# Kernel optimization log

Measured on AMD Instinct MI355X. Metric: run time of the kernel, lower is better.

The kernel has to match this reference:

```python
import jax, jax.numpy as jnp
import numpy as np

B, D_IMG, D_TXT, E = 4096, 768, 768, 512
LAMBDA_CMP = 1.0
EPS = 1e-10


def setup_inputs() -> dict:
    key = jax.random.key(0)
    k1, k2, k3, k4, k5 = jax.random.split(key, 5)
    return {
        "images": jax.random.normal(k1, (B, D_IMG), dtype=jnp.float32),
        "texts": jax.random.normal(k2, (B, D_TXT), dtype=jnp.float32),
        "labels": jax.random.randint(k3, (B,), 0, 1000, dtype=jnp.int32),
        "W_img": jax.random.normal(k4, (D_IMG, E), dtype=jnp.float32) / np.sqrt(D_IMG),
        "W_txt": jax.random.normal(k5, (D_TXT, E), dtype=jnp.float32) / np.sqrt(D_TXT),
        "logit_scale": jnp.asarray(np.log(1.0 / 0.07), dtype=jnp.float32),
    }


def reference(images, texts, labels, W_img, W_txt, logit_scale):
    # CLIP-style encoders: linear project + L2 normalize
    img = images @ W_img
    txt = texts @ W_txt
    img = img / jnp.linalg.norm(img, axis=-1, keepdims=True)
    txt = txt / jnp.linalg.norm(txt, axis=-1, keepdims=True)
    logits = jnp.exp(logit_scale) * (img @ txt.T)  # [B, B]

    b = logits.shape[0]
    rows = jnp.arange(b)
    logp = jax.nn.log_softmax(logits, axis=-1)
    clip_loss = -jnp.mean(logp[rows, labels])

    probs = jnp.exp(logp)                # softmax probs [B, B]
    p_yi = probs[rows, labels]           # [B]
    # columns j whose label differs from sample i's label AND prob exceeds p_yi
    diff_label = labels[None, :] != labels[:, None]           # [B, B]
    mask = diff_label & (probs > p_yi[:, None])               # [B, B]
    denom = jnp.sum(jnp.where(mask, probs, 0.0), axis=1)      # [B]
    has_any = jnp.any(mask, axis=1)
    cmp_loss = jnp.sum(jnp.where(has_any, p_yi / (denom + EPS), 0.0)) / b

    return clip_loss + LAMBDA_CMP * cmp_loss
```

## Files before the change

kernel.cpp:

```cpp
#include <hip/hip_runtime.h>
#include <stdint.h>

#define BATCH 4096
#define DDIM  768
#define EDIM  512
#define NS    64
#define LOG2E 1.44269504088896340736f

using short8  = __attribute__((ext_vector_type(8))) short;
using float4v = __attribute__((ext_vector_type(4))) float;

__device__ __forceinline__ unsigned short f2bf(float x) {
    union { float f; uint32_t u; } v; v.f = x;
    uint32_t u = v.u;
    u += 0x7FFFu + ((u >> 16) & 1u);
    return (unsigned short)(u >> 16);
}
__device__ __forceinline__ float bf2f(unsigned short h) {
    union { uint32_t u; float f; } v; v.u = ((uint32_t)h) << 16;
    return v.f;
}

__device__ __forceinline__ void gl2lds16(const void* g, void* l) {
    __builtin_amdgcn_global_load_lds(
        (const __attribute__((address_space(1))) void*)g,
        (__attribute__((address_space(3))) void*)l, 16, 0, 0);
}

__global__ void prep(const float* __restrict__ images, const float* __restrict__ texts,
                     const float* __restrict__ W_img, const float* __restrict__ W_txt,
                     unsigned short* __restrict__ img_bf, unsigned short* __restrict__ txt_bf,
                     unsigned short* __restrict__ wt_img, unsigned short* __restrict__ wt_txt) {
    __shared__ float tile[32][33];
    int bid = blockIdx.x;
    if (bid < 6144) {
        int which = bid >= 3072;
        int i = (bid - (which ? 3072 : 0)) * 256 + threadIdx.x;
        const float* in = which ? texts : images;
        unsigned short* out = which ? txt_bf : img_bf;
        float4 v = ((const float4*)in)[i];
        ushort4 o;
        o.x = f2bf(v.x); o.y = f2bf(v.y); o.z = f2bf(v.z); o.w = f2bf(v.w);
        ((ushort4*)out)[i] = o;
        return;
    }
    int tb = bid - 6144;
    int which = tb >= 384;
    if (which) tb -= 384;
    const float* W = which ? W_txt : W_img;
    unsigned short* Wt = which ? wt_txt : wt_img;
    int n0 = (tb & 15) * 32, k0 = (tb >> 4) * 32;
    int tid = threadIdx.x;
    for (int p = 0; p < 4; ++p) {
        int e = tid + p * 256; int lr = e >> 5, lc = e & 31;
        tile[lc][lr] = W[(size_t)(k0 + lr) * EDIM + n0 + lc];
    }
    __syncthreads();
    for (int p = 0; p < 4; ++p) {
        int e = tid + p * 256; int lr = e >> 5, lc = e & 31;
        Wt[(size_t)(n0 + lr) * DDIM + k0 + lc] = f2bf(tile[lr][lc]);
    }
}

__global__ __launch_bounds__(256) void gemm_nt(const unsigned short* __restrict__ Aimg,
                                               const unsigned short* __restrict__ Atxt,
                                               const unsigned short* __restrict__ Bimg,
                                               const unsigned short* __restrict__ Btxt,
                                               unsigned short* __restrict__ Cimg,
                                               unsigned short* __restrict__ Ctxt) {
    const unsigned short* A  = blockIdx.z ? Atxt : Aimg;
    const unsigned short* Bm = blockIdx.z ? Btxt : Bimg;
    unsigned short* C        = blockIdx.z ? Ctxt : Cimg;
    __shared__ __align__(16) unsigned short As[2][128 * 64];
    __shared__ __align__(16) unsigned short Bs[2][64 * 64];
    int tid = threadIdx.x;
    int wave = tid >> 6, lane = tid & 63;
    int q = lane >> 4, r = lane & 15;
    int m0 = blockIdx.x * 128, n0 = blockIdx.y * 64;
    int sw = (r >> 1) & 3;

    const unsigned short* gsA[4];
    unsigned short* lsA[4];
    for (int i = 0; i < 4; ++i) {
        int u = i * 256 + tid;
        int kc2 = u >> 9, row = (u >> 2) & 127, kq = u & 3;
        int kq2 = kq ^ ((row >> 1) & 3);
        gsA[i] = &A[(size_t)(m0 + row) * DDIM + kc2 * 32 + kq2 * 8];
        lsA[i] = &As[0][u * 8];
    }
    const unsigned short* gsB[2];
    unsigned short* lsB[2];
    for (int i = 0; i < 2; ++i) {
        int u = i * 256 + tid;
        int kc2 = u >> 8, row = (u >> 2) & 63, kq = u & 3;
        int kq2 = kq ^ ((row >> 1) & 3);
        gsB[i] = &Bm[(size_t)(n0 + row) * DDIM + kc2 * 32 + kq2 * 8];
        lsB[i] = &Bs[0][u * 8];
    }

    float4v acc[2][4];
    for (int a = 0; a < 2; ++a)
        for (int t = 0; t < 4; ++t) acc[a][t] = (float4v){0.f, 0.f, 0.f, 0.f};

    for (int i = 0; i < 4; ++i) gl2lds16(gsA[i], lsA[i]);
    for (int i = 0; i < 2; ++i) gl2lds16(gsB[i], lsB[i]);
    __syncthreads();

    for (int it = 0; it < DDIM / 64; ++it) {
        int b = it & 1;
        if (it < DDIM / 64 - 1) {
            int k0 = (it + 1) * 64;
            for (int i = 0; i < 4; ++i) gl2lds16(gsA[i] + k0, lsA[i] + (b ^ 1) * (128 * 64));
            for (int i = 0; i < 2; ++i) gl2lds16(gsB[i] + k0, lsB[i] + (b ^ 1) * (64 * 64));
        }
        for (int kc2 = 0; kc2 < 2; ++kc2) {
            short8 a0 = *(const short8*)&As[b][kc2 * 4096 + (wave * 32 + r) * 32 + (q ^ sw) * 8];
            short8 a1 = *(const short8*)&As[b][kc2 * 4096 + (wave * 32 + 16 + r) * 32 + (q ^ sw) * 8];
            for (int t = 0; t < 4; ++t) {
                short8 bfr = *(const short8*)&Bs[b][kc2 * 2048 + (t * 16 + r) * 32 + (q ^ sw) * 8];
                acc[0][t] = __builtin_amdgcn_mfma_f32_16x16x32_bf16(a0, bfr, acc[0][t], 0, 0, 0);
                acc[1][t] = __builtin_amdgcn_mfma_f32_16x16x32_bf16(a1, bfr, acc[1][t], 0, 0, 0);
            }
        }
        __syncthreads();
    }
    for (int rg = 0; rg < 2; ++rg)
        for (int t = 0; t < 4; ++t)
            for (int g = 0; g < 4; ++g)
                C[(size_t)(m0 + wave * 32 + rg * 16 + q * 4 + g) * EDIM + n0 + t * 16 + r] =
                    f2bf(acc[rg][t][g]);
}

__global__ void norm_rows(unsigned short* __restrict__ Pa, unsigned short* __restrict__ Pb) {
    unsigned short* P = blockIdx.y ? Pb : Pa;
    int wave = threadIdx.x >> 6, lane = threadIdx.x & 63;
    int row = blockIdx.x * 4 + wave;
    unsigned short* p = &P[(size_t)row * 512 + lane * 8];
    union { unsigned short us[8]; uint4 u4; } v;
    v.u4 = *(const uint4*)p;
    float f[8], s = 0.f;
    for (int j = 0; j < 8; ++j) { f[j] = bf2f(v.us[j]); s += f[j] * f[j]; }
    for (int off = 1; off < 64; off <<= 1) s += __shfl_xor(s, off);
    float rn = rsqrtf(s);
    for (int j = 0; j < 8; ++j) v.us[j] = f2bf(f[j] * rn);
    *(uint4*)p = v.u4;
}

__global__ void tdot(const unsigned short* __restrict__ img, const unsigned short* __restrict__ txt,
                     const int* __restrict__ labels, float* __restrict__ tout) {
    int wave = threadIdx.x >> 6, lane = threadIdx.x & 63;
    int row = blockIdx.x * 4 + wave;
    int lab = labels[row];
    union { unsigned short us[8]; uint4 u4; } a, b;
    a.u4 = *(const uint4*)&img[(size_t)row * 512 + lane * 8];
    b.u4 = *(const uint4*)&txt[(size_t)lab * 512 + lane * 8];
    float s = 0.f;
    for (int j = 0; j < 8; ++j) s += bf2f(a.us[j]) * bf2f(b.us[j]);
    for (int off = 1; off < 64; off <<= 1) s += __shfl_xor(s, off);
    if (lane == 0) tout[row] = s;
}

__global__ __launch_bounds__(256) void flash_pass(
    const unsigned short* __restrict__ img, const unsigned short* __restrict__ txt,
    const int* __restrict__ labels, const float* __restrict__ tvals,
    const float* __restrict__ ls,
    float* __restrict__ lP, float* __restrict__ dP) {
    __shared__ __align__(16) unsigned short As[2][128 * 64];
    __shared__ __align__(16) unsigned short Bs[2][128 * 64];
    int tid = threadIdx.x;
    int wave = tid >> 6, lane = tid & 63;
    int wr = wave >> 1, wc = wave & 1;
    int q = lane >> 4, r = lane & 15;
    int n0 = blockIdx.x * 128;
    int m0 = blockIdx.y * 128;
    float alpha = expf(ls[0]);
    float c1 = alpha * LOG2E;
    int sw = (r >> 1) & 3;

    const unsigned short* gsA[4]; const unsigned short* gsB[4];
    unsigned short *lsA[4], *lsB[4];
    for (int i = 0; i < 4; ++i) {
        int u = i * 256 + tid;
        int kc2 = u >> 9, row = (u >> 2) & 127, kq = u & 3;
        int kq2 = kq ^ ((row >> 1) & 3);
        gsA[i] = &img[(size_t)(m0 + row) * 512 + kc2 * 32 + kq2 * 8];
        gsB[i] = &txt[(size_t)(n0 + row) * 512 + kc2 * 32 + kq2 * 8];
        lsA[i] = &As[0][u * 8];
        lsB[i] = &Bs[0][u * 8];
    }

    float4v acc[4][4];
    #pragma unroll
    for (int st = 0; st < 4; ++st)
        #pragma unroll
        for (int cf = 0; cf < 4; ++cf) acc[st][cf] = (float4v){0.f, 0.f, 0.f, 0.f};

    for (int i = 0; i < 4; ++i) gl2lds16(gsA[i], lsA[i]);
    for (int i = 0; i < 4; ++i) gl2lds16(gsB[i], lsB[i]);
    __syncthreads();

    for (int it = 0; it < 8; ++it) {
        int b = it & 1;
        if (it < 7) {
            int k0 = (it + 1) * 64;
            for (int i = 0; i < 4; ++i) gl2lds16(gsA[i] + k0, lsA[i] + (b ^ 1) * (128 * 64));
            for (int i = 0; i < 4; ++i) gl2lds16(gsB[i] + k0, lsB[i] + (b ^ 1) * (128 * 64));
        }
        #pragma unroll
        for (int kc2 = 0; kc2 < 2; ++kc2) {
            short8 av[4], bv[4];
            #pragma unroll
            for (int st = 0; st < 4; ++st)
                av[st] = *(const short8*)&As[b][kc2 * 4096 + (wr * 64 + st * 16 + r) * 32 + (q ^ sw) * 8];
            #pragma unroll
            for (int cf = 0; cf < 4; ++cf)
                bv[cf] = *(const short8*)&Bs[b][kc2 * 4096 + (wc * 64 + cf * 16 + r) * 32 + (q ^ sw) * 8];
            #pragma unroll
            for (int st = 0; st < 4; ++st)
                #pragma unroll
                for (int cf = 0; cf < 4; ++cf)
                    acc[st][cf] = __builtin_amdgcn_mfma_f32_16x16x32_bf16(av[st], bv[cf],
                                                                          acc[st][cf], 0, 0, 0);
        }
        __syncthreads();
    }

    int lc[4];
    #pragma unroll
    for (int cf = 0; cf < 4; ++cf) lc[cf] = labels[n0 + wc * 64 + cf * 16 + r];
    int cb = blockIdx.x * 2 + wc;
    #pragma unroll
    for (int st = 0; st < 4; ++st) {
        int labr[4]; float tr[4];
        #pragma unroll
        for (int g = 0; g < 4; ++g) {
            int rw = m0 + wr * 64 + st * 16 + q * 4 + g;
            labr[g] = labels[rw];
            tr[g] = tvals[rw];
        }
        float l4[4] = {0.f, 0.f, 0.f, 0.f}, d4[4] = {0.f, 0.f, 0.f, 0.f};
        #pragma unroll
        for (int cf = 0; cf < 4; ++cf)
            #pragma unroll
            for (int g = 0; g < 4; ++g) {
                float a = acc[st][cf][g];
                float p = exp2f(fmaf(a, c1, -c1));
                l4[g] += p;
                d4[g] += ((a > tr[g]) && (lc[cf] != labr[g])) ? p : 0.f;
            }
        #pragma unroll
        for (int g = 0; g < 4; ++g) {
            float lv = l4[g], dv = d4[g];
            for (int off = 1; off < 16; off <<= 1) {
                lv += __shfl_xor(lv, off);
                dv += __shfl_xor(dv, off);
            }
            if (r == 0) {
                int rw = m0 + wr * 64 + st * 16 + q * 4 + g;
                lP[(size_t)rw * NS + cb] = lv;
                dP[(size_t)rw * NS + cb] = dv;
            }
        }
    }
}

__global__ void combine(const float* __restrict__ lP, const float* __restrict__ dP,
                        const float* __restrict__ tvals, const float* __restrict__ ls,
                        float* __restrict__ out) {
    int row = blockIdx.x * 256 + threadIdx.x;
    float alpha = expf(ls[0]);
    float L = 0.f, D = 0.f;
    for (int s = 0; s < NS; ++s) {
        L += lP[(size_t)row * NS + s];
        D += dP[(size_t)row * NS + s];
    }
    float tm = alpha * (tvals[row] - 1.0f);
    float clip = logf(L) - tm;
    float py = expf(tm) / L;
    float cmp = (D > 0.f) ? py / (D / L + 1e-10f) : 0.f;
    float v = clip + cmp;
    for (int off = 1; off < 64; off <<= 1) v += __shfl_xor(v, off);
    __shared__ float w4[4];
    int wave = threadIdx.x >> 6, lane = threadIdx.x & 63;
    if (lane == 0) w4[wave] = v;
    __syncthreads();
    if (threadIdx.x == 0)
        atomicAdd(out, (w4[0] + w4[1] + w4[2] + w4[3]) * (1.0f / BATCH));
}

extern "C" void kernel_launch(void* const* d_in, const int* in_sizes, int n_in,
                              void* d_out, int out_size, void* d_ws, size_t ws_size,
                              hipStream_t stream) {
    const float* images = (const float*)d_in[0];
    const float* texts  = (const float*)d_in[1];
    const int*   labels = (const int*)d_in[2];
    const float* W_img  = (const float*)d_in[3];
    const float* W_txt  = (const float*)d_in[4];
    const float* lscale = (const float*)d_in[5];
    float* out = (float*)d_out;

    char* ws = (char*)d_ws;
    unsigned short* img_bf = (unsigned short*)(ws + 0);
    unsigned short* txt_bf = (unsigned short*)(ws + 6291456);
    unsigned short* wt_img = (unsigned short*)(ws + 12582912);
    unsigned short* wt_txt = (unsigned short*)(ws + 13369344);
    unsigned short* proj_i = (unsigned short*)(ws + 14155776);
    unsigned short* proj_t = (unsigned short*)(ws + 18350080);
    float*          lP     = (float*)(ws + 0);
    float*          dP     = (float*)(ws + 1048576);
    float*          tvals  = (float*)(ws + 2097152);

    hipMemsetAsync(out, 0, sizeof(float), stream);
    prep<<<6912, 256, 0, stream>>>(images, texts, W_img, W_txt, img_bf, txt_bf, wt_img, wt_txt);
    gemm_nt<<<dim3(BATCH / 128, EDIM / 64, 2), 256, 0, stream>>>(img_bf, txt_bf, wt_img, wt_txt,
                                                                 proj_i, proj_t);
    norm_rows<<<dim3(BATCH / 4, 2), 256, 0, stream>>>(proj_i, proj_t);
    tdot<<<BATCH / 4, 256, 0, stream>>>(proj_i, proj_t, labels, tvals);
    flash_pass<<<dim3(BATCH / 128, BATCH / 128), 256, 0, stream>>>(proj_i, proj_t, labels, tvals,
                                                                   lscale, lP, dP);
    combine<<<16, 256, 0, stream>>>(lP, dP, tvals, lscale, out);
}
```

Before: 141.0 us.

## Enlarge flash_pass tile to 256x256 with 8 waves and interleaved prefetch schedule

Grows the logits tile per block from 128x128 to 256x256 and the block from 4 to 8 waves, so each wave now accumulates a 128x64 output slice. The K loop is split into four MFMA phases, each with its own LDS fragment loads, part of the next-tile global-to-LDS prefetch, explicit barriers and raised wave priority. The aim is more reuse per LDS byte and better overlap of memory traffic with MFMA work. The cost is 128KB of LDS per block and a grid of only 256 blocks, which allows one block per CU and gives no tail slack.

```diff
diff --git a/kernel.cpp b/kernel.cpp
--- a/kernel.cpp
+++ b/kernel.cpp
@@ -160,81 +160,154 @@
     if (lane == 0) tout[row] = s;
 }
 
-__global__ __launch_bounds__(256) void flash_pass(
+__global__ __launch_bounds__(512) void flash_pass(
     const unsigned short* __restrict__ img, const unsigned short* __restrict__ txt,
     const int* __restrict__ labels, const float* __restrict__ tvals,
     const float* __restrict__ ls,
     float* __restrict__ lP, float* __restrict__ dP) {
-    __shared__ __align__(16) unsigned short As[2][128 * 64];
-    __shared__ __align__(16) unsigned short Bs[2][128 * 64];
+    __shared__ __align__(16) unsigned short As[2][16384];
+    __shared__ __align__(16) unsigned short Bs[2][16384];
     int tid = threadIdx.x;
     int wave = tid >> 6, lane = tid & 63;
-    int wr = wave >> 1, wc = wave & 1;
+    int wr = wave >> 2, wc = wave & 3;
     int q = lane >> 4, r = lane & 15;
-    int n0 = blockIdx.x * 128;
-    int m0 = blockIdx.y * 128;
+    int n0 = blockIdx.x * 256;
+    int m0 = blockIdx.y * 256;
     float alpha = expf(ls[0]);
     float c1 = alpha * LOG2E;
     int sw = (r >> 1) & 3;
 
-    const unsigned short* gsA[4]; const unsigned short* gsB[4];
-    unsigned short *lsA[4], *lsB[4];
+    int soff[4], slds[4];
     for (int i = 0; i < 4; ++i) {
-        int u = i * 256 + tid;
-        int kc2 = u >> 9, row = (u >> 2) & 127, kq = u & 3;
+        int u = i * 512 + tid;
+        int kc2 = u >> 10, row = (u >> 2) & 255, kq = u & 3;
         int kq2 = kq ^ ((row >> 1) & 3);
-        gsA[i] = &img[(size_t)(m0 + row) * 512 + kc2 * 32 + kq2 * 8];
-        gsB[i] = &txt[(size_t)(n0 + row) * 512 + kc2 * 32 + kq2 * 8];
-        lsA[i] = &As[0][u * 8];
-        lsB[i] = &Bs[0][u * 8];
-    }
-
-    float4v acc[4][4];
-    #pragma unroll
-    for (int st = 0; st < 4; ++st)
-        #pragma unroll
-        for (int cf = 0; cf < 4; ++cf) acc[st][cf] = (float4v){0.f, 0.f, 0.f, 0.f};
-
-    for (int i = 0; i < 4; ++i) gl2lds16(gsA[i], lsA[i]);
-    for (int i = 0; i < 4; ++i) gl2lds16(gsB[i], lsB[i]);
-    __syncthreads();
-
-    for (int it = 0; it < 8; ++it) {
-        int b = it & 1;
-        if (it < 7) {
-            int k0 = (it + 1) * 64;
-            for (int i = 0; i < 4; ++i) gl2lds16(gsA[i] + k0, lsA[i] + (b ^ 1) * (128 * 64));
-            for (int i = 0; i < 4; ++i) gl2lds16(gsB[i] + k0, lsB[i] + (b ^ 1) * (128 * 64));
-        }
-        #pragma unroll
-        for (int kc2 = 0; kc2 < 2; ++kc2) {
-            short8 av[4], bv[4];
-            #pragma unroll
-            for (int st = 0; st < 4; ++st)
-                av[st] = *(const short8*)&As[b][kc2 * 4096 + (wr * 64 + st * 16 + r) * 32 + (q ^ sw) * 8];
-            #pragma unroll
-            for (int cf = 0; cf < 4; ++cf)
-                bv[cf] = *(const short8*)&Bs[b][kc2 * 4096 + (wc * 64 + cf * 16 + r) * 32 + (q ^ sw) * 8];
-            #pragma unroll
-            for (int st = 0; st < 4; ++st)
+        soff[i] = row * 512 + kc2 * 32 + kq2 * 8;
+        slds[i] = u * 8;
+    }
+    const unsigned short* gA = img + (size_t)m0 * 512;
+    const unsigned short* gB = txt + (size_t)n0 * 512;
+
+    float4v acc[8][4];
+    #pragma unroll
+    for (int s = 0; s < 8; ++s)
+        #pragma unroll
+        for (int c = 0; c < 4; ++c) acc[s][c] = (float4v){0.f, 0.f, 0.f, 0.f};
+
+    #pragma unroll
+    for (int i = 0; i < 4; ++i) gl2lds16(gA + soff[i], &As[0][slds[i]]);
+    #pragma unroll
+    for (int i = 0; i < 4; ++i) gl2lds16(gB + soff[i], &Bs[0][slds[i]]);
+    asm volatile("s_waitcnt vmcnt(0)" ::: "memory");
+    __builtin_amdgcn_s_barrier();
+
+    short8 av[4][2];
+    short8 bv[2][2][2];
+
+    for (int kt = 0; kt < 8; ++kt) {
+        const unsigned short* As_ = &As[kt & 1][0];
+        const unsigned short* Bs_ = &Bs[kt & 1][0];
+        unsigned short* Asn = &As[(kt & 1) ^ 1][0];
+        unsigned short* Bsn = &Bs[(kt & 1) ^ 1][0];
+        int kn = (kt + 1) * 64;
+        bool pf = kt < 7;
+
+        #pragma unroll
+        for (int s = 0; s < 4; ++s)
+            #pragma unroll
+            for (int k = 0; k < 2; ++k)
+                av[s][k] = *(const short8*)&As_[k * 8192 + (wr * 128 + s * 16 + r) * 32 + (q ^ sw) * 8];
+        #pragma unroll
+        for (int j = 0; j < 2; ++j)
+            #pragma unroll
+            for (int k = 0; k < 2; ++k)
+                bv[0][j][k] = *(const short8*)&Bs_[k * 8192 + (wc * 64 + j * 16 + r) * 32 + (q ^ sw) * 8];
+        if (pf) { gl2lds16(gA + kn + soff[0], Asn + slds[0]);
+                  gl2lds16(gA + kn + soff[1], Asn + slds[1]); }
+        __builtin_amdgcn_sched_barrier(0);
+        __builtin_amdgcn_s_barrier();
+        __builtin_amdgcn_s_setprio(1);
+        #pragma unroll
+        for (int s = 0; s < 4; ++s)
+            #pragma unroll
+            for (int j = 0; j < 2; ++j)
                 #pragma unroll
-                for (int cf = 0; cf < 4; ++cf)
-                    acc[st][cf] = __builtin_amdgcn_mfma_f32_16x16x32_bf16(av[st], bv[cf],
-                                                                          acc[st][cf], 0, 0, 0);
-        }
-        __syncthreads();
+                for (int k = 0; k < 2; ++k)
+                    acc[s][j] = __builtin_amdgcn_mfma_f32_16x16x32_bf16(av[s][k], bv[0][j][k],
+                                                                        acc[s][j], 0, 0, 0);
+        __builtin_amdgcn_s_setprio(0);
+        __builtin_amdgcn_s_barrier();
+
+        #pragma unroll
+        for (int j = 0; j < 2; ++j)
+            #pragma unroll
+            for (int k = 0; k < 2; ++k)
+                bv[1][j][k] = *(const short8*)&Bs_[k * 8192 + (wc * 64 + 32 + j * 16 + r) * 32 + (q ^ sw) * 8];
+        if (pf) { gl2lds16(gA + kn + soff[2], Asn + slds[2]);
+                  gl2lds16(gA + kn + soff[3], Asn + slds[3]); }
+        __builtin_amdgcn_sched_barrier(0);
+        __builtin_amdgcn_s_barrier();
+        __builtin_amdgcn_s_setprio(1);
+        #pragma unroll
+        for (int s = 0; s < 4; ++s)
+            #pragma unroll
+            for (int j = 0; j < 2; ++j)
+                #pragma unroll
+                for (int k = 0; k < 2; ++k)
+                    acc[s][2 + j] = __builtin_amdgcn_mfma_f32_16x16x32_bf16(av[s][k], bv[1][j][k],
+                                                                            acc[s][2 + j], 0, 0, 0);
+        __builtin_amdgcn_s_setprio(0);
+        __builtin_amdgcn_s_barrier();
+
+        #pragma unroll
+        for (int s = 0; s < 4; ++s)
+            #pragma unroll
+            for (int k = 0; k < 2; ++k)
+                av[s][k] = *(const short8*)&As_[k * 8192 + (wr * 128 + 64 + s * 16 + r) * 32 + (q ^ sw) * 8];
+        if (pf) { gl2lds16(gB + kn + soff[0], Bsn + slds[0]);
+                  gl2lds16(gB + kn + soff[1], Bsn + slds[1]); }
+        __builtin_amdgcn_sched_barrier(0);
+        __builtin_amdgcn_s_barrier();
+        __builtin_amdgcn_s_setprio(1);
+        #pragma unroll
+        for (int s = 0; s < 4; ++s)
+            #pragma unroll
+            for (int j = 0; j < 2; ++j)
+                #pragma unroll
+                for (int k = 0; k < 2; ++k)
+                    acc[4 + s][j] = __builtin_amdgcn_mfma_f32_16x16x32_bf16(av[s][k], bv[0][j][k],
+                                                                            acc[4 + s][j], 0, 0, 0);
+        __builtin_amdgcn_s_setprio(0);
+        __builtin_amdgcn_s_barrier();
+
+        if (pf) { gl2lds16(gB + kn + soff[2], Bsn + slds[2]);
+                  gl2lds16(gB + kn + soff[3], Bsn + slds[3]); }
+        __builtin_amdgcn_sched_barrier(0);
+        __builtin_amdgcn_s_barrier();
+        __builtin_amdgcn_s_setprio(1);
+        #pragma unroll
+        for (int s = 0; s < 4; ++s)
+            #pragma unroll
+            for (int j = 0; j < 2; ++j)
+                #pragma unroll
+                for (int k = 0; k < 2; ++k)
+                    acc[4 + s][2 + j] = __builtin_amdgcn_mfma_f32_16x16x32_bf16(av[s][k], bv[1][j][k],
+                                                                                acc[4 + s][2 + j], 0, 0, 0);
+        __builtin_amdgcn_s_setprio(0);
+        asm volatile("s_waitcnt vmcnt(0)" ::: "memory");
+        __builtin_amdgcn_s_barrier();
     }
 
     int lc[4];
     #pragma unroll
     for (int cf = 0; cf < 4; ++cf) lc[cf] = labels[n0 + wc * 64 + cf * 16 + r];
-    int cb = blockIdx.x * 2 + wc;
-    #pragma unroll
-    for (int st = 0; st < 4; ++st) {
+    int cb = blockIdx.x * 4 + wc;
+    #pragma unroll
+    for (int st = 0; st < 8; ++st) {
         int labr[4]; float tr[4];
         #pragma unroll
         for (int g = 0; g < 4; ++g) {
-            int rw = m0 + wr * 64 + st * 16 + q * 4 + g;
+            int rw = m0 + wr * 128 + st * 16 + q * 4 + g;
             labr[g] = labels[rw];
             tr[g] = tvals[rw];
         }
@@ -256,7 +329,7 @@
                 dv += __shfl_xor(dv, off);
             }
             if (r == 0) {
-                int rw = m0 + wr * 64 + st * 16 + q * 4 + g;
+                int rw = m0 + wr * 128 + st * 16 + q * 4 + g;
                 lP[(size_t)rw * NS + cb] = lv;
                 dP[(size_t)rw * NS + cb] = dv;
             }
@@ -316,7 +389,7 @@
                                                                  proj_i, proj_t);
     norm_rows<<<dim3(BATCH / 4, 2), 256, 0, stream>>>(proj_i, proj_t);
     tdot<<<BATCH / 4, 256, 0, stream>>>(proj_i, proj_t, labels, tvals);
-    flash_pass<<<dim3(BATCH / 128, BATCH / 128), 256, 0, stream>>>(proj_i, proj_t, labels, tvals,
+    flash_pass<<<dim3(BATCH / 256, BATCH / 256), 512, 0, stream>>>(proj_i, proj_t, labels, tvals,
                                                                    lscale, lP, dP);
     combine<<<16, 256, 0, stream>>>(lP, dP, tvals, lscale, out);
 }
```

New measurement: 139.5 us. No clear change (-1.1%).
